# Kernel tuning notes

Hardware: AMD Instinct MI355X
Metric: run time of the kernel (lower is better)

Reference implementation:

```python
import jax, jax.numpy as jnp
import numpy as np

D_MAIN = 256
D_INT = 512
N_FEAT = 128
N_CLASSES = 10
B = 1024
N_CAND = 100000
CTX = 96
EPS = 1e-5


def layer_norm(x, scale, bias):
    m = jnp.mean(x, axis=-1, keepdims=True)
    v = jnp.var(x, axis=-1, keepdims=True)
    return (x - m) / jnp.sqrt(v + EPS) * scale + bias


def setup_inputs() -> dict:
    key = jax.random.key(0)
    ks = jax.random.split(key, 16)

    def lin_w(k, fi, fo):
        return jax.random.uniform(k, (fi, fo), minval=-1.0, maxval=1.0, dtype=jnp.float32) / np.sqrt(fi)

    def lin_b(k, fi, fo):
        return jax.random.uniform(k, (fo,), minval=-1.0, maxval=1.0, dtype=jnp.float32) / np.sqrt(fi)

    return {
        "x_num": jax.random.normal(ks[0], (B, N_FEAT), dtype=jnp.float32),
        "cand_num": jax.random.normal(ks[1], (N_CAND, N_FEAT), dtype=jnp.float32),
        "cand_y": jax.random.randint(ks[2], (N_CAND,), 0, N_CLASSES),
        "context_size": CTX,
        # input linear (forward_E with encoder_n_blocks=0)
        "W_lin": lin_w(ks[3], N_FEAT, D_MAIN), "b_lin": lin_b(ks[3], N_FEAT, D_MAIN),
        # K projection
        "W_K": lin_w(ks[4], D_MAIN, D_MAIN), "b_K": lin_b(ks[4], D_MAIN, D_MAIN),
        # label embedding Y (init uniform(-1, 1) per reset_parameters)
        "Y_emb": jax.random.uniform(ks[5], (N_CLASSES, D_MAIN), minval=-1.0, maxval=1.0, dtype=jnp.float32),
        # T: Linear(d, d_int) -> ReLU -> Linear(d_int, d, bias=False)
        "T_W1": lin_w(ks[6], D_MAIN, D_INT), "T_b1": lin_b(ks[6], D_MAIN, D_INT),
        "T_W2": lin_w(ks[7], D_INT, D_MAIN),
        # predictor block (LayerNorm -> Linear -> ReLU -> Dropout -> Linear), residual
        "bp_ln_s": jnp.ones((D_MAIN,), jnp.float32), "bp_ln_b": jnp.zeros((D_MAIN,), jnp.float32),
        "bp_W1": lin_w(ks[8], D_MAIN, D_INT), "bp_b1": lin_b(ks[8], D_MAIN, D_INT),
        "bp_W2": lin_w(ks[9], D_INT, D_MAIN), "bp_b2": lin_b(ks[9], D_INT, D_MAIN),
        # head P: LayerNorm -> ReLU -> Linear(d, n_classes)
        "P_ln_s": jnp.ones((D_MAIN,), jnp.float32), "P_ln_b": jnp.zeros((D_MAIN,), jnp.float32),
        "P_W": lin_w(ks[10], D_MAIN, N_CLASSES), "P_b": lin_b(ks[10], D_MAIN, N_CLASSES),
    }


def reference(x_num, cand_num, cand_y, context_size,
              W_lin, b_lin, W_K, b_K, Y_emb, T_W1, T_b1, T_W2,
              bp_ln_s, bp_ln_b, bp_W1, bp_b1, bp_W2, bp_b2,
              P_ln_s, P_ln_b, P_W, P_b):
    # forward_E (encoder_n_blocks=0 => single Linear, normlization is None)
    x = x_num @ W_lin + b_lin                       # [B, d]
    k = x @ W_K + b_K                               # [B, d]

    # candidate keys computed under torch.no_grad in the original -> stop_gradient
    ki_all = jax.lax.stop_gradient((cand_num @ W_lin + b_lin) @ W_K + b_K)  # [N, d]

    # FAISS GpuIndexFlatL2 search: exact L2 top-k (smallest squared distance)
    d2 = (jnp.sum(k * k, axis=-1, keepdims=True)
          - 2.0 * (k @ ki_all.T)
          + jnp.sum(ki_all * ki_all, axis=-1))      # [B, N]
    _, I = jax.lax.top_k(-jax.lax.stop_gradient(d2), context_size)  # [B, C]

    ki = ki_all[I]                                  # [B, C, d]
    diff = k[:, None, :] - ki                       # [B, C, d]
    # NOTE: source computes S = -(-|k|^2 + 2 k.ki - |ki|^2) = +squared distance
    S = jnp.sum(diff * diff, axis=-1)               # [B, C]
    w = jax.nn.softmax(S, axis=-1)                  # context_dropout inactive at inference

    enc_y = Y_emb[cand_y[I]]                        # [B, C, d]
    V = enc_y + jax.nn.relu(diff @ T_W1 + T_b1) @ T_W2
    V = jnp.einsum('bc,bcd->bd', w, V)              # weighted aggregation

    x = x + V
    # predictor block (predictor_n_blocks=1)
    h = layer_norm(x, bp_ln_s, bp_ln_b)
    h = jax.nn.relu(h @ bp_W1 + bp_b1) @ bp_W2 + bp_b2
    x = x + h
    # head P
    return jax.nn.relu(layer_norm(x, P_ln_s, P_ln_b)) @ P_W + P_b
```

## Files before the change

### kernel.cpp

```cpp
#include <hip/hip_runtime.h>
#include <hip/hip_bf16.h>

#define B_ROWS   1024
#define N_FEAT   128
#define D_MAIN   256
#define D_INT    512
#define N_CAND   100000
#define CTX      96
#define N_CLS    10
#define PCHN     8192
#define N2       91808
#define RKEEP    128
#define SCAP     6144
#define SVSTRIDE 16

typedef __attribute__((ext_vector_type(8))) short bf16x8;
typedef __attribute__((ext_vector_type(4))) float f32x4;
typedef unsigned long long u64;

__device__ __forceinline__ float wsum(float v) {
    #pragma unroll
    for (int o = 32; o > 0; o >>= 1) v += __shfl_down(v, o);
    return v;
}
__device__ __forceinline__ float wmax(float v) {
    #pragma unroll
    for (int o = 32; o > 0; o >>= 1) v = fmaxf(v, __shfl_down(v, o));
    return v;
}
__device__ __forceinline__ float blockSum256(float v, float* red) {
    int t = threadIdx.x;
    float s = wsum(v);
    if ((t & 63) == 0) red[t >> 6] = s;
    __syncthreads();
    s = red[0] + red[1] + red[2] + red[3];
    __syncthreads();
    return s;
}
__device__ __forceinline__ float b2f(unsigned short u) {
    return __uint_as_float(((unsigned)u) << 16);
}
__device__ __forceinline__ unsigned short f2b(float f) {
    unsigned x = __float_as_uint(f);
    return (unsigned short)((x + 0x7fff + ((x >> 16) & 1)) >> 16);
}
__device__ __forceinline__ unsigned fkey(float f) {
    unsigned u = __float_as_uint(f);
    return u ^ ((((int)u >> 31)) | 0x80000000u);
}
__device__ __forceinline__ float finv(unsigned k) {
    unsigned u = (k & 0x80000000u) ? (k ^ 0x80000000u) : ~k;
    return __uint_as_float(u);
}
#define SPLIT1(x, hv, lv) { unsigned short _h = f2b(x); hv = (short)_h; lv = (short)f2b((x) - b2f(_h)); }

__global__ __launch_bounds__(256) void encode_batch(
    const float* __restrict__ xn, const float* __restrict__ Wl, const float* __restrict__ bl,
    const float* __restrict__ Wk, const float* __restrict__ bk,
    float* __restrict__ xout, float* __restrict__ kout, float* __restrict__ knorm)
{
    int b = blockIdx.x, t = threadIdx.x;
    __shared__ float si[128], sx[256], red[4];
    if (t < 128) si[t] = xn[b * N_FEAT + t];
    __syncthreads();
    float a = bl[t];
    for (int i = 0; i < 128; ++i) a += si[i] * Wl[i * D_MAIN + t];
    xout[b * D_MAIN + t] = a;
    sx[t] = a;
    __syncthreads();
    float a2 = bk[t];
    for (int i = 0; i < 256; ++i) a2 += sx[i] * Wk[i * D_MAIN + t];
    kout[b * D_MAIN + t] = a2;
    float s = blockSum256(a2 * a2, red);
    if (t == 0) knorm[b] = s;
}

__global__ __launch_bounds__(256) void fuse_weights(
    const float* __restrict__ Wl, const float* __restrict__ Wk,
    const float* __restrict__ bl, const float* __restrict__ bk,
    float* __restrict__ Wf, float* __restrict__ bf)
{
    int i = blockIdx.x, t = threadIdx.x;
    __shared__ float row[256];
    if (i < 128) {
        row[t] = Wl[i * D_MAIN + t];
        __syncthreads();
        float a = 0.f;
        for (int k = 0; k < 256; ++k) a += row[k] * Wk[k * D_MAIN + t];
        Wf[i * D_MAIN + t] = a;
    } else {
        row[t] = bl[t];
        __syncthreads();
        float a = bk[t];
        for (int k = 0; k < 256; ++k) a += row[k] * Wk[k * D_MAIN + t];
        bf[t] = a;
    }
}

template<bool WRITE_BF16>
__global__ __launch_bounds__(256) void gemm_split3(
    const float* __restrict__ A,
    const unsigned short* __restrict__ Bh,
    const unsigned short* __restrict__ Bl,
    const float* __restrict__ bias,
    float* __restrict__ Cf,
    unsigned short* __restrict__ Cbf,
    int M, int N, int K)
{
    __shared__ __align__(16) short Ash[4096], Asl[4096];
    __shared__ __align__(16) short Bsh[2048], Bsl[2048];
    const int t = threadIdx.x;
    const int bm = blockIdx.x * 128, bn = blockIdx.y * 64;
    const int wave = t >> 6, lane = t & 63;
    const int wm = (wave >> 1) * 64, wn = (wave & 1) * 32;
    const int lr = lane & 15, lkg = lane >> 4;
    f32x4 acc[4][2] = {};
    const int row0 = t >> 2, kg0 = t & 3;
    const int row1 = row0 + 64;
    const int p0 = ((kg0 + (row0 >> 2)) & 3) ^ (row0 & 3);
    const int p1 = ((kg0 + (row1 >> 2)) & 3) ^ (row1 & 3);
    const int gm0 = bm + row0, gm1 = bm + row1;
    const int nB = bn + row0;

    float4 u00, u01, u10, u11;
    bf16x8 bh0, bl0;
    auto prefetch = [&](int kq) {
        float4 z4 = make_float4(0.f, 0.f, 0.f, 0.f); bf16x8 z = {};
        u00 = z4; u01 = z4; u10 = z4; u11 = z4;
        bh0 = z; bl0 = z;
        if (gm0 < M) {
            const float* ap = A + (size_t)gm0 * K + kq + kg0 * 8;
            u00 = *(const float4*)ap; u01 = *(const float4*)(ap + 4);
        }
        if (gm1 < M) {
            const float* ap = A + (size_t)gm1 * K + kq + kg0 * 8;
            u10 = *(const float4*)ap; u11 = *(const float4*)(ap + 4);
        }
        if (nB < N) {
            bh0 = *(const bf16x8*)(Bh + (size_t)nB * K + kq + kg0 * 8);
            bl0 = *(const bf16x8*)(Bl + (size_t)nB * K + kq + kg0 * 8);
        }
    };
    prefetch(0);

    for (int k0 = 0; k0 < K; k0 += 32) {
        bf16x8 a0h, a0l, a1h, a1l;
        SPLIT1(u00.x, a0h[0], a0l[0]); SPLIT1(u00.y, a0h[1], a0l[1]);
        SPLIT1(u00.z, a0h[2], a0l[2]); SPLIT1(u00.w, a0h[3], a0l[3]);
        SPLIT1(u01.x, a0h[4], a0l[4]); SPLIT1(u01.y, a0h[5], a0l[5]);
        SPLIT1(u01.z, a0h[6], a0l[6]); SPLIT1(u01.w, a0h[7], a0l[7]);
        SPLIT1(u10.x, a1h[0], a1l[0]); SPLIT1(u10.y, a1h[1], a1l[1]);
        SPLIT1(u10.z, a1h[2], a1l[2]); SPLIT1(u10.w, a1h[3], a1l[3]);
        SPLIT1(u11.x, a1h[4], a1l[4]); SPLIT1(u11.y, a1h[5], a1l[5]);
        SPLIT1(u11.z, a1h[6], a1l[6]); SPLIT1(u11.w, a1h[7], a1l[7]);
        __syncthreads();
        *(bf16x8*)&Ash[(row0 * 4 + p0) * 8] = a0h;
        *(bf16x8*)&Asl[(row0 * 4 + p0) * 8] = a0l;
        *(bf16x8*)&Ash[(row1 * 4 + p1) * 8] = a1h;
        *(bf16x8*)&Asl[(row1 * 4 + p1) * 8] = a1l;
        *(bf16x8*)&Bsh[(row0 * 4 + p0) * 8] = bh0;
        *(bf16x8*)&Bsl[(row0 * 4 + p0) * 8] = bl0;
        if (k0 + 32 < K) prefetch(k0 + 32);
        __syncthreads();
        bf16x8 bfh[2], bfl[2];
        #pragma unroll
        for (int n = 0; n < 2; ++n) {
            int r = wn + n * 16 + lr;
            int p = ((lkg + (r >> 2)) & 3) ^ (r & 3);
            bfh[n] = *(const bf16x8*)&Bsh[(r * 4 + p) * 8];
            bfl[n] = *(const bf16x8*)&Bsl[(r * 4 + p) * 8];
        }
        #pragma unroll
        for (int m = 0; m < 4; ++m) {
            int r = wm + m * 16 + lr;
            int p = ((lkg + (r >> 2)) & 3) ^ (r & 3);
            bf16x8 ah = *(const bf16x8*)&Ash[(r * 4 + p) * 8];
            bf16x8 al = *(const bf16x8*)&Asl[(r * 4 + p) * 8];
            #pragma unroll
            for (int n = 0; n < 2; ++n) {
                acc[m][n] = __builtin_amdgcn_mfma_f32_16x16x32_bf16(al, bfh[n], acc[m][n], 0, 0, 0);
                acc[m][n] = __builtin_amdgcn_mfma_f32_16x16x32_bf16(ah, bfl[n], acc[m][n], 0, 0, 0);
                acc[m][n] = __builtin_amdgcn_mfma_f32_16x16x32_bf16(ah, bfh[n], acc[m][n], 0, 0, 0);
            }
        }
    }
    #pragma unroll
    for (int m = 0; m < 4; ++m) {
        #pragma unroll
        for (int n = 0; n < 2; ++n) {
            f32x4 a = acc[m][n];
            int gcol = bn + wn + n * 16 + lr;
            if (gcol >= N) continue;
            float bv = bias[gcol];
            #pragma unroll
            for (int r = 0; r < 4; ++r) {
                int grow = bm + wm + m * 16 + lkg * 4 + r;
                if (grow >= M) continue;
                float v = a[r] + bv;
                Cf[(size_t)grow * N + gcol] = v;
                if (WRITE_BF16) Cbf[(size_t)grow * N + gcol] = f2b(v);
            }
        }
    }
}

template<bool RELU, bool OUT_BF16>
__global__ __launch_bounds__(256) void gemm_bf16(
    const unsigned short* __restrict__ A,
    const unsigned short* __restrict__ Bt,
    const float* __restrict__ bias,
    void* __restrict__ C, int M, int N, int K)
{
    __shared__ __align__(16) short As[2][4096];
    __shared__ __align__(16) short Bs[2][2048];
    const int t = threadIdx.x;
    const int bm = blockIdx.x * 128, bn = blockIdx.y * 64;
    const int wave = t >> 6, lane = t & 63;
    const int wm = (wave >> 1) * 64, wn = (wave & 1) * 32;
    const int lr = lane & 15, lkg = lane >> 4;
    f32x4 acc[4][2] = {};
    const int row0 = t >> 2, kg0 = t & 3;
    const int row1 = row0 + 64;
    const int p0 = ((kg0 + (row0 >> 2)) & 3) ^ (row0 & 3);
    const int p1 = ((kg0 + (row1 >> 2)) & 3) ^ (row1 & 3);
    const int gm0 = bm + row0, gm1 = bm + row1;
    const int nB = bn + row0;

    bf16x8 a0, a1, b0;
    auto prefetch = [&](int kq) {
        bf16x8 z = {};
        a0 = z; a1 = z; b0 = z;
        if (gm0 < M) a0 = *(const bf16x8*)(A + (size_t)gm0 * K + kq + kg0 * 8);
        if (gm1 < M) a1 = *(const bf16x8*)(A + (size_t)gm1 * K + kq + kg0 * 8);
        if (nB < N) b0 = *(const bf16x8*)(Bt + (size_t)nB * K + kq + kg0 * 8);
    };
    prefetch(0);
    *(bf16x8*)&As[0][(row0 * 4 + p0) * 8] = a0;
    *(bf16x8*)&As[0][(row1 * 4 + p1) * 8] = a1;
    *(bf16x8*)&Bs[0][(row0 * 4 + p0) * 8] = b0;
    if (32 < K) prefetch(32);
    __syncthreads();

    for (int k0 = 0; k0 < K; k0 += 32) {
        const int cur = (k0 >> 5) & 1;
        if (k0 + 32 < K) {
            const int nxt = cur ^ 1;
            *(bf16x8*)&As[nxt][(row0 * 4 + p0) * 8] = a0;
            *(bf16x8*)&As[nxt][(row1 * 4 + p1) * 8] = a1;
            *(bf16x8*)&Bs[nxt][(row0 * 4 + p0) * 8] = b0;
            if (k0 + 64 < K) prefetch(k0 + 64);
        }
        bf16x8 bfr[2];
        #pragma unroll
        for (int n = 0; n < 2; ++n) {
            int r = wn + n * 16 + lr;
            int p = ((lkg + (r >> 2)) & 3) ^ (r & 3);
            bfr[n] = *(const bf16x8*)&Bs[cur][(r * 4 + p) * 8];
        }
        #pragma unroll
        for (int m = 0; m < 4; ++m) {
            int r = wm + m * 16 + lr;
            int p = ((lkg + (r >> 2)) & 3) ^ (r & 3);
            bf16x8 af = *(const bf16x8*)&As[cur][(r * 4 + p) * 8];
            #pragma unroll
            for (int n = 0; n < 2; ++n)
                acc[m][n] = __builtin_amdgcn_mfma_f32_16x16x32_bf16(
                    af, bfr[n], acc[m][n], 0, 0, 0);
        }
        __syncthreads();
    }
    #pragma unroll
    for (int m = 0; m < 4; ++m) {
        #pragma unroll
        for (int n = 0; n < 2; ++n) {
            f32x4 a = acc[m][n];
            int gcol = bn + wn + n * 16 + lr;
            if (gcol >= N) continue;
            float bv = bias ? bias[gcol] : 0.f;
            #pragma unroll
            for (int r = 0; r < 4; ++r) {
                int grow = bm + wm + m * 16 + lkg * 4 + r;
                if (grow >= M) continue;
                float v = a[r] + bv;
                if (RELU) v = fmaxf(v, 0.f);
                if (OUT_BF16)
                    ((unsigned short*)C)[(size_t)grow * N + gcol] = f2b(v);
                else
                    ((float*)C)[(size_t)grow * N + gcol] = v;
            }
        }
    }
}

template<int MODE>
__global__ __launch_bounds__(256) void screen_gemm(
    const unsigned short* __restrict__ A,
    const unsigned short* __restrict__ Bt,
    float* __restrict__ scores,
    int N, int n0,
    const float* __restrict__ knrm,
    const unsigned* __restrict__ tau32, int* __restrict__ svcnt,
    u64* __restrict__ surv)
{
    __shared__ __align__(16) short As[2][4096];
    __shared__ __align__(16) short Bs[2][2048];
    const int t = threadIdx.x;
    const int bm = blockIdx.x * 128, bn = blockIdx.y * 64;
    const int wave = t >> 6, lane = t & 63;
    const int wm = (wave >> 1) * 64, wn = (wave & 1) * 32;
    const int lr = lane & 15, lkg = lane >> 4;
    f32x4 acc[4][2] = {};
    const int row0 = t >> 2, kg0 = t & 3;
    const int row1 = row0 + 64;
    const int p0 = ((kg0 + (row0 >> 2)) & 3) ^ (row0 & 3);
    const int p1 = ((kg0 + (row1 >> 2)) & 3) ^ (row1 & 3);
    const int gm0 = bm + row0, gm1 = bm + row1;
    const int nB = bn + row0;

    bf16x8 a0, a1, b0;
    auto prefetch = [&](int kq) {
        bf16x8 z = {};
        b0 = z;
        a0 = *(const bf16x8*)(A + (size_t)gm0 * D_MAIN + kq + kg0 * 8);
        a1 = *(const bf16x8*)(A + (size_t)gm1 * D_MAIN + kq + kg0 * 8);
        if (nB < N) b0 = *(const bf16x8*)(Bt + (size_t)nB * D_MAIN + kq + kg0 * 8);
    };
    prefetch(0);
    *(bf16x8*)&As[0][(row0 * 4 + p0) * 8] = a0;
    *(bf16x8*)&As[0][(row1 * 4 + p1) * 8] = a1;
    *(bf16x8*)&Bs[0][(row0 * 4 + p0) * 8] = b0;
    prefetch(32);
    __syncthreads();

    for (int k0 = 0; k0 < D_MAIN; k0 += 32) {
        const int cur = (k0 >> 5) & 1;
        if (k0 + 32 < D_MAIN) {
            const int nxt = cur ^ 1;
            *(bf16x8*)&As[nxt][(row0 * 4 + p0) * 8] = a0;
            *(bf16x8*)&As[nxt][(row1 * 4 + p1) * 8] = a1;
            *(bf16x8*)&Bs[nxt][(row0 * 4 + p0) * 8] = b0;
            if (k0 + 64 < D_MAIN) prefetch(k0 + 64);
        }
        bf16x8 bfr[2];
        #pragma unroll
        for (int n = 0; n < 2; ++n) {
            int r = wn + n * 16 + lr;
            int p = ((lkg + (r >> 2)) & 3) ^ (r & 3);
            bfr[n] = *(const bf16x8*)&Bs[cur][(r * 4 + p) * 8];
        }
        #pragma unroll
        for (int m = 0; m < 4; ++m) {
            int r = wm + m * 16 + lr;
            int p = ((lkg + (r >> 2)) & 3) ^ (r & 3);
            bf16x8 af = *(const bf16x8*)&As[cur][(r * 4 + p) * 8];
            #pragma unroll
            for (int n = 0; n < 2; ++n)
                acc[m][n] = __builtin_amdgcn_mfma_f32_16x16x32_bf16(
                    af, bfr[n], acc[m][n], 0, 0, 0);
        }
        __syncthreads();
    }

    float knv[2];
    #pragma unroll
    for (int n = 0; n < 2; ++n) {
        int gcol = bn + wn + n * 16 + lr;
        knv[n] = (gcol < N) ? knrm[gcol] : 0.f;
    }
    if (MODE == 1) {
        #pragma unroll
        for (int m = 0; m < 4; ++m) {
            #pragma unroll
            for (int n = 0; n < 2; ++n) {
                int gcol = bn + wn + n * 16 + lr;
                if (gcol >= N) continue;
                #pragma unroll
                for (int r = 0; r < 4; ++r) {
                    int grow = bm + wm + m * 16 + lkg * 4 + r;
                    scores[(size_t)grow * PCHN + gcol] = knv[n] - 2.0f * acc[m][n][r];
                }
            }
        }
    } else {
        unsigned taur[16];
        #pragma unroll
        for (int m = 0; m < 4; ++m)
            #pragma unroll
            for (int r = 0; r < 4; ++r)
                taur[m * 4 + r] = tau32[bm + wm + m * 16 + lkg * 4 + r];
        #pragma unroll
        for (int m = 0; m < 4; ++m) {
            #pragma unroll
            for (int r = 0; r < 4; ++r) {
                int grow = bm + wm + m * 16 + lkg * 4 + r;
                #pragma unroll
                for (int n = 0; n < 2; ++n) {
                    int gcol = bn + wn + n * 16 + lr;
                    bool pass = false;
                    unsigned key = 0;
                    if (gcol < N) {
                        key = fkey(knv[n] - 2.0f * acc[m][n][r]);
                        pass = key <= taur[m * 4 + r];
                    }
                    u64 bal = __ballot(pass);
                    unsigned g16 = (unsigned)((bal >> (lkg * 16)) & 0xFFFFu);
                    if (g16) {
                        int cntp = __popc(g16);
                        int first = __ffs(g16) - 1;
                        int base = 0;
                        if (lr == first) base = atomicAdd(&svcnt[grow * SVSTRIDE], cntp);
                        base = __shfl(base, lkg * 16 + first);
                        if (pass) {
                            int p = base + __popc(g16 & ((1u << lr) - 1u));
                            if (p < SCAP)
                                surv[(size_t)grow * SCAP + p] =
                                    ((u64)key << 32) | (unsigned)(n0 + gcol);
                        }
                    }
                }
            }
        }
    }
}

__global__ __launch_bounds__(256) void cvt_f32_bf16_vec(
    const float* __restrict__ in, unsigned short* __restrict__ out, int n4)
{
    int i = blockIdx.x * 256 + threadIdx.x;
    if (i >= n4) return;
    float4 v = ((const float4*)in)[i];
    ushort4 u;
    u.x = f2b(v.x); u.y = f2b(v.y); u.z = f2b(v.z); u.w = f2b(v.w);
    ((ushort4*)out)[i] = u;
}
__global__ __launch_bounds__(256) void cvt_transpose(
    const float* __restrict__ W, unsigned short* __restrict__ Wt, int K, int N)
{
    int idx = blockIdx.x * 256 + threadIdx.x;
    if (idx >= K * N) return;
    int k = idx / N, n = idx % N;
    Wt[(size_t)n * K + k] = f2b(W[idx]);
}
__global__ __launch_bounds__(256) void cvt_split_transpose(
    const float* __restrict__ W, unsigned short* __restrict__ Wh,
    unsigned short* __restrict__ Wl, int K, int N)
{
    int idx = blockIdx.x * 256 + threadIdx.x;
    if (idx >= K * N) return;
    int k = idx / N, n = idx % N;
    float v = W[idx];
    unsigned short h = f2b(v);
    Wh[(size_t)n * K + k] = h;
    Wl[(size_t)n * K + k] = f2b(v - b2f(h));
}

__global__ __launch_bounds__(256) void rownorms(const float* __restrict__ ki,
                                                float* __restrict__ out, int M)
{
    int n = blockIdx.x * 4 + (threadIdx.x >> 6);
    int lane = threadIdx.x & 63;
    if (n >= M) return;
    float4 v = *(const float4*)(ki + (size_t)n * D_MAIN + lane * 4);
    float s = v.x * v.x + v.y * v.y + v.z * v.z + v.w * v.w;
    s = wsum(s);
    if (lane == 0) out[n] = s;
}

__device__ void bitonic512(u64* s, int t)
{
    for (int k = 2; k <= 512; k <<= 1) {
        for (int j = k >> 1; j > 0; j >>= 1) {
            __syncthreads();
            #pragma unroll
            for (int q = 0; q < 2; ++q) {
                int l = t + q * 256;
                int p = l ^ j;
                if (p > l) {
                    u64 a = s[l], bb = s[p];
                    bool up = ((l & k) == 0);
                    if ((a > bb) == up) { s[l] = bb; s[p] = a; }
                }
            }
        }
    }
    __syncthreads();
}
__device__ void bitonic1024(u64* s, int t)
{
    for (int k = 2; k <= 1024; k <<= 1) {
        for (int j = k >> 1; j > 0; j >>= 1) {
            __syncthreads();
            #pragma unroll
            for (int q = 0; q < 4; ++q) {
                int l = t + q * 256;
                int p = l ^ j;
                if (p > l) {
                    u64 a = s[l], bb = s[p];
                    bool up = ((l & k) == 0);
                    if ((a > bb) == up) { s[l] = bb; s[p] = a; }
                }
            }
        }
    }
    __syncthreads();
}

__global__ __launch_bounds__(256) void pilot_select(
    const float* __restrict__ scores, u64* __restrict__ pilotbuf,
    unsigned* __restrict__ tau32)
{
    int b = blockIdx.x, t = threadIdx.x;
    int lane = t & 63;
    __shared__ u64 s[1024];
    __shared__ int cnt;
    __shared__ u64 tauf;
    const float* row = scores + (size_t)b * PCHN;
    #pragma unroll
    for (int q = 0; q < 4; ++q) {
        int n = t + q * 256;
        s[n] = ((u64)fkey(row[n]) << 32) | (unsigned)n;
    }
    __syncthreads();
    bitonic1024(s, t);
    if (t == 0) { cnt = 128; tauf = s[127]; }
    #pragma unroll
    for (int q = 0; q < 4; ++q) { int n = t + q * 256; if (n >= 128) s[n] = ~0ULL; }
    __syncthreads();
    for (int base = 1024; base < PCHN; base += 1024) {
        u64 tau = tauf;
        int n = base + t * 4;
        float4 v = *(const float4*)(row + n);
        #pragma unroll
        for (int j = 0; j < 4; ++j) {
            float x = (&v.x)[j];
            u64 e = ((u64)fkey(x) << 32) | (unsigned)(n + j);
            bool pass = e < tau;
            u64 m = __ballot(pass);
            if (m) {
                int bs = 0;
                if (lane == 0) bs = atomicAdd(&cnt, (int)__popcll(m));
                bs = __shfl(bs, 0);
                if (pass) {
                    int p = bs + (int)__popcll(m & ((1ULL << lane) - 1ULL));
                    if (p < 1024) s[p] = e;
                }
            }
        }
        __syncthreads();
        if (cnt > 512) {
            bitonic1024(s, t);
            if (t == 0) { cnt = 128; tauf = s[127]; }
            #pragma unroll
            for (int q = 0; q < 4; ++q) { int n2 = t + q * 256; if (n2 >= 128) s[n2] = ~0ULL; }
        }
        __syncthreads();
    }
    bitonic1024(s, t);
    if (t < 128) pilotbuf[(size_t)b * 128 + t] = s[t];
    if (t == 0) tau32[b] = (unsigned)(s[127] >> 32);
}

__global__ __launch_bounds__(128) void init_surv(
    const u64* __restrict__ pilotbuf, u64* __restrict__ surv, int* __restrict__ svcnt)
{
    int b = blockIdx.x, t = threadIdx.x;
    surv[(size_t)b * SCAP + t] = pilotbuf[(size_t)b * 128 + t];
    if (t == 0) svcnt[b * SVSTRIDE] = 128;
}

__global__ __launch_bounds__(256) void final_select(
    const u64* __restrict__ surv, const int* __restrict__ svcnt,
    int* __restrict__ refI)
{
    int b = blockIdx.x, t = threadIdx.x;
    int lane = t & 63;
    __shared__ u64 s[1024];
    __shared__ int cnt;
    __shared__ u64 tauf;
    int total = svcnt[b * SVSTRIDE]; if (total > SCAP) total = SCAP;
    const u64* rowp = surv + (size_t)b * SCAP;
    #pragma unroll
    for (int q = 0; q < 4; ++q) {
        int n = t + q * 256;
        s[n] = (n < total) ? rowp[n] : ~0ULL;
    }
    __syncthreads();
    bitonic1024(s, t);
    if (t == 0) { cnt = 128; tauf = s[127]; }
    #pragma unroll
    for (int q = 0; q < 4; ++q) { int n = t + q * 256; if (n >= 128) s[n] = ~0ULL; }
    __syncthreads();
    for (int base = 1024; base < total; base += 1024) {
        u64 tau = tauf;
        int n = base + t * 4;
        #pragma unroll
        for (int j = 0; j < 4; ++j) {
            u64 e = (n + j < total) ? rowp[n + j] : ~0ULL;
            bool pass = e < tau;
            u64 m = __ballot(pass);
            if (m) {
                int bs = 0;
                if (lane == 0) bs = atomicAdd(&cnt, (int)__popcll(m));
                bs = __shfl(bs, 0);
                if (pass) {
                    int p = bs + (int)__popcll(m & ((1ULL << lane) - 1ULL));
                    if (p < 1024) s[p] = e;
                }
            }
        }
        __syncthreads();
        if (cnt > 512) {
            bitonic1024(s, t);
            if (t == 0) { cnt = 128; tauf = s[127]; }
            #pragma unroll
            for (int q = 0; q < 4; ++q) { int n2 = t + q * 256; if (n2 >= 128) s[n2] = ~0ULL; }
        }
        __syncthreads();
    }
    bitonic1024(s, t);
    if (t < RKEEP) refI[b * RKEEP + t] = (int)(unsigned)(s[t] & 0xffffffffULL);
}

__global__ __launch_bounds__(256) void refine(
    const float* __restrict__ kmat, const float* __restrict__ kiall,
    const float* __restrict__ knorm, const float* __restrict__ kinorm,
    const int* __restrict__ refI, int* __restrict__ Ifin, float* __restrict__ Sbuf)
{
    int b = blockIdx.x, t = threadIdx.x;
    int w = t >> 6, lane = t & 63;
    __shared__ float kk[256];
    __shared__ u64 s[512];
    kk[t] = kmat[b * D_MAIN + t];
    s[t] = ~0ULL; s[t + 256] = ~0ULL;
    __syncthreads();
    float kn = knorm[b];
    for (int sv = w; sv < RKEEP; sv += 4) {
        int n = refI[b * RKEEP + sv];
        float4 a = *(const float4*)&kk[lane * 4];
        float4 bb = ((const float4*)(kiall + (size_t)n * D_MAIN))[lane];
        float d = a.x * bb.x + a.y * bb.y + a.z * bb.z + a.w * bb.w;
        d = wsum(d);
        if (lane == 0) {
            float d2 = kn + kinorm[n] - 2.f * d;
            s[sv] = ((u64)fkey(d2) << 32) | (unsigned)n;
        }
    }
    __syncthreads();
    bitonic512(s, t);
    if (t < CTX) {
        u64 e = s[t];
        Ifin[b * CTX + t] = (int)(unsigned)(e & 0xffffffffULL);
        Sbuf[b * CTX + t] = finv((unsigned)(e >> 32));
    }
}

__global__ __launch_bounds__(64) void gather_diff_bf(
    const float* __restrict__ kmat, const float* __restrict__ kiall,
    const int* __restrict__ I, unsigned short* __restrict__ diffb)
{
    int bc = blockIdx.x;
    int b = bc / CTX;
    int t = threadIdx.x;
    int idx = I[bc];
    float4 kv = ((const float4*)(kmat + (size_t)b * D_MAIN))[t];
    float4 iv = ((const float4*)(kiall + (size_t)idx * D_MAIN))[t];
    ushort4 u;
    u.x = f2b(kv.x - iv.x); u.y = f2b(kv.y - iv.y);
    u.z = f2b(kv.z - iv.z); u.w = f2b(kv.w - iv.w);
    ((ushort4*)(diffb + (size_t)bc * D_MAIN))[t] = u;
}

__global__ __launch_bounds__(128) void softmax96(const float* __restrict__ S,
                                                 float* __restrict__ w)
{
    int b = blockIdx.x, t = threadIdx.x;
    __shared__ float rm[2], rs[2];
    float v = (t < CTX) ? S[b * CTX + t] : -__builtin_inff();
    float m = wmax(v);
    if ((t & 63) == 0) rm[t >> 6] = m;
    __syncthreads();
    m = fmaxf(rm[0], rm[1]);
    float e = (t < CTX) ? expf(v - m) : 0.f;
    float ss = wsum(e);
    if ((t & 63) == 0) rs[t >> 6] = ss;
    __syncthreads();
    float Z = rs[0] + rs[1];
    if (t < CTX) w[b * CTX + t] = e / Z;
}

__global__ __launch_bounds__(256) void aggregate(
    const float* __restrict__ w, const int* __restrict__ I,
    const int* __restrict__ cand_y, const float* __restrict__ Yemb,
    const float* __restrict__ mlp, const float* __restrict__ x,
    float* __restrict__ x2)
{
    int b = blockIdx.x, t = threadIdx.x;
    __shared__ float ws[CTX];
    __shared__ int lab[CTX];
    if (t < CTX) {
        ws[t] = w[b * CTX + t];
        lab[t] = cand_y[I[b * CTX + t]];
    }
    __syncthreads();
    float acc = 0.f;
    for (int c = 0; c < CTX; ++c) {
        acc += ws[c] * (Yemb[lab[c] * D_MAIN + t] + mlp[((size_t)b * CTX + c) * D_MAIN + t]);
    }
    x2[b * D_MAIN + t] = x[b * D_MAIN + t] + acc;
}

__global__ __launch_bounds__(256) void predictor_head(
    const float* __restrict__ x2,
    const float* __restrict__ lns, const float* __restrict__ lnb,
    const float* __restrict__ W1, const float* __restrict__ b1,
    const float* __restrict__ W2, const float* __restrict__ b2,
    const float* __restrict__ plns, const float* __restrict__ plnb,
    const float* __restrict__ PW, const float* __restrict__ Pb,
    float* __restrict__ out)
{
    int b = blockIdx.x, t = threadIdx.x;
    __shared__ float ln1[256], hdn[512], red[4];
    float xv = x2[b * D_MAIN + t];
    float s1 = blockSum256(xv, red);
    float s2 = blockSum256(xv * xv, red);
    float mean = s1 * (1.f / 256.f);
    float var = s2 * (1.f / 256.f) - mean * mean;
    float rstd = rsqrtf(var + 1e-5f);
    ln1[t] = (xv - mean) * rstd * lns[t] + lnb[t];
    __syncthreads();
    #pragma unroll
    for (int rep = 0; rep < 2; ++rep) {
        int j = t + rep * 256;
        float a = b1[j];
        for (int i = 0; i < 256; ++i) a += ln1[i] * W1[i * D_INT + j];
        hdn[j] = fmaxf(a, 0.f);
    }
    __syncthreads();
    float a3 = b2[t];
    for (int i = 0; i < 512; ++i) a3 += hdn[i] * W2[i * D_MAIN + t];
    float x3 = xv + a3;
    float s3 = blockSum256(x3, red);
    float s4 = blockSum256(x3 * x3, red);
    float m2 = s3 * (1.f / 256.f);
    float v2 = s4 * (1.f / 256.f) - m2 * m2;
    float r2 = rsqrtf(v2 + 1e-5f);
    float rv = fmaxf((x3 - m2) * r2 * plns[t] + plnb[t], 0.f);
    __syncthreads();
    ln1[t] = rv;
    __syncthreads();
    if (t < N_CLS) {
        float a = Pb[t];
        for (int i = 0; i < 256; ++i) a += ln1[i] * PW[i * N_CLS + t];
        out[b * N_CLS + t] = a;
    }
}

extern "C" void kernel_launch(void* const* d_in, const int* in_sizes, int n_in,
                              void* d_out, int out_size, void* d_ws, size_t ws_size,
                              hipStream_t stream)
{
    (void)in_sizes; (void)n_in; (void)out_size; (void)ws_size;
    const float* x_num   = (const float*)d_in[0];
    const float* cand    = (const float*)d_in[1];
    const int*   cand_y  = (const int*)d_in[2];
    const float* W_lin   = (const float*)d_in[4];
    const float* b_lin   = (const float*)d_in[5];
    const float* W_K     = (const float*)d_in[6];
    const float* b_K     = (const float*)d_in[7];
    const float* Y_emb   = (const float*)d_in[8];
    const float* T_W1    = (const float*)d_in[9];
    const float* T_b1    = (const float*)d_in[10];
    const float* T_W2    = (const float*)d_in[11];
    const float* bp_ln_s = (const float*)d_in[12];
    const float* bp_ln_b = (const float*)d_in[13];
    const float* bp_W1   = (const float*)d_in[14];
    const float* bp_b1   = (const float*)d_in[15];
    const float* bp_W2   = (const float*)d_in[16];
    const float* bp_b2   = (const float*)d_in[17];
    const float* P_ln_s  = (const float*)d_in[18];
    const float* P_ln_b  = (const float*)d_in[19];
    const float* P_W     = (const float*)d_in[20];
    const float* P_b     = (const float*)d_in[21];
    float* outp = (float*)d_out;

    char* ws = (char*)d_ws;
    float* kiall  = (float*)(ws + 0);
    unsigned short* hidden = (unsigned short*)(ws + 0);
    unsigned short* ki_bf = (unsigned short*)(ws + 102400000);
    unsigned short* diffb = (unsigned short*)(ws + 102400000);
    float* mlpbuf = (float*)(ws + 102400000);
    float* scores = (float*)(ws + 153600000);
    u64*   surv   = (u64*)(ws + 153600000);
    const size_t T = 204800000;
    float* xbuf   = (float*)(ws + T + 0);
    float* kbuf   = (float*)(ws + T + 1048576);
    float* x2buf  = (float*)(ws + T + 2097152);
    float* knorm  = (float*)(ws + T + 3145728);
    float* kinorm = (float*)(ws + T + 3149824);
    unsigned short* k_bf = (unsigned short*)(ws + T + 3551232);
    float* Wf     = (float*)(ws + T + 4075520);
    unsigned short* WfH = (unsigned short*)(ws + T + 4206592);
    unsigned short* WfL = (unsigned short*)(ws + T + 4272128);
    float* bfused = (float*)(ws + T + 4337664);
    unsigned short* W1t  = (unsigned short*)(ws + T + 4468736);
    unsigned short* W2t  = (unsigned short*)(ws + T + 4730880);
    float* Sbuf   = (float*)(ws + T + 4993024);
    float* wbuf   = (float*)(ws + T + 5386240);
    int*   refI   = (int*)(ws + T + 5779456);
    int*   Ifin   = (int*)(ws + T + 6303744);
    u64*   pilotbuf = (u64*)(ws + T + 6696960);
    unsigned* tau32 = (unsigned*)(ws + T + 7745536);
    int*   svcnt  = (int*)(ws + T + 7749632);

    encode_batch<<<B_ROWS, 256, 0, stream>>>(x_num, W_lin, b_lin, W_K, b_K,
                                             xbuf, kbuf, knorm);
    fuse_weights<<<129, 256, 0, stream>>>(W_lin, W_K, b_lin, b_K, Wf, bfused);
    cvt_split_transpose<<<128, 256, 0, stream>>>(Wf, WfH, WfL, N_FEAT, D_MAIN);
    cvt_transpose<<<512, 256, 0, stream>>>(T_W1, W1t, D_MAIN, D_INT);
    cvt_transpose<<<512, 256, 0, stream>>>(T_W2, W2t, D_INT, D_MAIN);
    cvt_f32_bf16_vec<<<256, 256, 0, stream>>>(kbuf, k_bf, B_ROWS * D_MAIN / 4);
    gemm_split3<true><<<dim3(782, 4), 256, 0, stream>>>(
        cand, WfH, WfL, bfused, kiall, ki_bf, N_CAND, D_MAIN, N_FEAT);
    rownorms<<<25000, 256, 0, stream>>>(kiall, kinorm, N_CAND);
    screen_gemm<1><<<dim3(8, PCHN / 64), 256, 0, stream>>>(
        k_bf, ki_bf, scores, PCHN, 0, kinorm, nullptr, nullptr, nullptr);
    pilot_select<<<B_ROWS, 256, 0, stream>>>(scores, pilotbuf, tau32);
    init_surv<<<B_ROWS, 128, 0, stream>>>(pilotbuf, surv, svcnt);
    screen_gemm<2><<<dim3(8, (N2 + 63) / 64), 256, 0, stream>>>(
        k_bf, ki_bf + (size_t)PCHN * D_MAIN, nullptr, N2, PCHN,
        kinorm + PCHN, tau32, svcnt, surv);
    final_select<<<B_ROWS, 256, 0, stream>>>(surv, svcnt, refI);
    refine<<<B_ROWS, 256, 0, stream>>>(kbuf, kiall, knorm, kinorm, refI, Ifin, Sbuf);
    softmax96<<<B_ROWS, 128, 0, stream>>>(Sbuf, wbuf);
    gather_diff_bf<<<B_ROWS * CTX, 64, 0, stream>>>(kbuf, kiall, Ifin, diffb);
    gemm_bf16<true, true><<<dim3(768, 8), 256, 0, stream>>>(
        diffb, W1t, T_b1, hidden, B_ROWS * CTX, D_INT, D_MAIN);
    gemm_bf16<false, false><<<dim3(768, 4), 256, 0, stream>>>(
        hidden, W2t, nullptr, mlpbuf, B_ROWS * CTX, D_MAIN, D_INT);
    aggregate<<<B_ROWS, 256, 0, stream>>>(wbuf, Ifin, cand_y, Y_emb, mlpbuf,
                                          xbuf, x2buf);
    predictor_head<<<B_ROWS, 256, 0, stream>>>(x2buf, bp_ln_s, bp_ln_b,
                                               bp_W1, bp_b1, bp_W2, bp_b2,
                                               P_ln_s, P_ln_b, P_W, P_b, outp);
}
```

Measured before the change: 802.1 us.

## Stage GEMM tiles via direct global-to-LDS async loads

Replaces the register-staged prefetch and LDS store in both the generic bf16 GEMM and the screening GEMM with global_load_lds 16-byte direct transfers. An inverse-swizzle mapping picks each lane's source chunk so the existing swizzled LDS layout stays the same. This is meant to cut VGPR pressure and the LDS write instructions in the main loop. Out-of-bounds guards on M/N are dropped, so partial tiles (e.g. the candidate tail) may read past the array end. Whether the async loads are properly waited on before the barrier is also uncertain.

```diff
diff --git a/kernel.cpp b/kernel.cpp
--- a/kernel.cpp
+++ b/kernel.cpp
@@ -51,6 +51,13 @@
 __device__ __forceinline__ float finv(unsigned k) {
     unsigned u = (k & 0x80000000u) ? (k ^ 0x80000000u) : ~k;
     return __uint_as_float(u);
+}
+__device__ __forceinline__ void async16(const unsigned short* g, short* l) {
+    __builtin_amdgcn_global_load_lds((const unsigned int*)g, (unsigned int*)l, 16, 0, 0);
+}
+__device__ __forceinline__ int inv_kg(int s) {
+    int g = s >> 2;
+    return (((s & 3) ^ (g & 3)) - (g >> 2)) & 3;
 }
 #define SPLIT1(x, hv, lv) { unsigned short _h = f2b(x); hv = (short)_h; lv = (short)f2b((x) - b2f(_h)); }
 
@@ -219,37 +226,24 @@
     const int wm = (wave >> 1) * 64, wn = (wave & 1) * 32;
     const int lr = lane & 15, lkg = lane >> 4;
     f32x4 acc[4][2] = {};
-    const int row0 = t >> 2, kg0 = t & 3;
-    const int row1 = row0 + 64;
-    const int p0 = ((kg0 + (row0 >> 2)) & 3) ^ (row0 & 3);
-    const int p1 = ((kg0 + (row1 >> 2)) & 3) ^ (row1 & 3);
-    const int gm0 = bm + row0, gm1 = bm + row1;
-    const int nB = bn + row0;
-
-    bf16x8 a0, a1, b0;
-    auto prefetch = [&](int kq) {
-        bf16x8 z = {};
-        a0 = z; a1 = z; b0 = z;
-        if (gm0 < M) a0 = *(const bf16x8*)(A + (size_t)gm0 * K + kq + kg0 * 8);
-        if (gm1 < M) a1 = *(const bf16x8*)(A + (size_t)gm1 * K + kq + kg0 * 8);
-        if (nB < N) b0 = *(const bf16x8*)(Bt + (size_t)nB * K + kq + kg0 * 8);
+
+    const int sA0 = wave * 128 + lane, sA1 = sA0 + 64, sB = wave * 64 + lane;
+    const unsigned short* srcA0 = A + (size_t)(bm + (sA0 >> 2)) * K + inv_kg(sA0) * 8;
+    const unsigned short* srcA1 = A + (size_t)(bm + (sA1 >> 2)) * K + inv_kg(sA1) * 8;
+    const unsigned short* srcB  = Bt + (size_t)(bn + (sB >> 2)) * K + inv_kg(sB) * 8;
+
+    auto stage = [&](int buf, int kq) {
+        async16(srcA0 + kq, &As[buf][(wave * 128) * 8]);
+        async16(srcA1 + kq, &As[buf][(wave * 128 + 64) * 8]);
+        async16(srcB + kq, &Bs[buf][(wave * 64) * 8]);
     };
-    prefetch(0);
-    *(bf16x8*)&As[0][(row0 * 4 + p0) * 8] = a0;
-    *(bf16x8*)&As[0][(row1 * 4 + p1) * 8] = a1;
-    *(bf16x8*)&Bs[0][(row0 * 4 + p0) * 8] = b0;
-    if (32 < K) prefetch(32);
-    __syncthreads();
-
-    for (int k0 = 0; k0 < K; k0 += 32) {
-        const int cur = (k0 >> 5) & 1;
-        if (k0 + 32 < K) {
-            const int nxt = cur ^ 1;
-            *(bf16x8*)&As[nxt][(row0 * 4 + p0) * 8] = a0;
-            *(bf16x8*)&As[nxt][(row1 * 4 + p1) * 8] = a1;
-            *(bf16x8*)&Bs[nxt][(row0 * 4 + p0) * 8] = b0;
-            if (k0 + 64 < K) prefetch(k0 + 64);
-        }
+    stage(0, 0);
+    __syncthreads();
+
+    const int nsteps = K >> 5;
+    for (int s = 0; s < nsteps; ++s) {
+        const int cur = s & 1;
+        if (s + 1 < nsteps) stage(cur ^ 1, (s + 1) << 5);
         bf16x8 bfr[2];
         #pragma unroll
         for (int n = 0; n < 2; ++n) {
@@ -310,37 +304,23 @@
     const int wm = (wave >> 1) * 64, wn = (wave & 1) * 32;
     const int lr = lane & 15, lkg = lane >> 4;
     f32x4 acc[4][2] = {};
-    const int row0 = t >> 2, kg0 = t & 3;
-    const int row1 = row0 + 64;
-    const int p0 = ((kg0 + (row0 >> 2)) & 3) ^ (row0 & 3);
-    const int p1 = ((kg0 + (row1 >> 2)) & 3) ^ (row1 & 3);
-    const int gm0 = bm + row0, gm1 = bm + row1;
-    const int nB = bn + row0;
-
-    bf16x8 a0, a1, b0;
-    auto prefetch = [&](int kq) {
-        bf16x8 z = {};
-        b0 = z;
-        a0 = *(const bf16x8*)(A + (size_t)gm0 * D_MAIN + kq + kg0 * 8);
-        a1 = *(const bf16x8*)(A + (size_t)gm1 * D_MAIN + kq + kg0 * 8);
-        if (nB < N) b0 = *(const bf16x8*)(Bt + (size_t)nB * D_MAIN + kq + kg0 * 8);
+
+    const int sA0 = wave * 128 + lane, sA1 = sA0 + 64, sB = wave * 64 + lane;
+    const unsigned short* srcA0 = A + (size_t)(bm + (sA0 >> 2)) * D_MAIN + inv_kg(sA0) * 8;
+    const unsigned short* srcA1 = A + (size_t)(bm + (sA1 >> 2)) * D_MAIN + inv_kg(sA1) * 8;
+    const unsigned short* srcB  = Bt + (size_t)(bn + (sB >> 2)) * D_MAIN + inv_kg(sB) * 8;
+
+    auto stage = [&](int buf, int kq) {
+        async16(srcA0 + kq, &As[buf][(wave * 128) * 8]);
+        async16(srcA1 + kq, &As[buf][(wave * 128 + 64) * 8]);
+        async16(srcB + kq, &Bs[buf][(wave * 64) * 8]);
     };
-    prefetch(0);
-    *(bf16x8*)&As[0][(row0 * 4 + p0) * 8] = a0;
-    *(bf16x8*)&As[0][(row1 * 4 + p1) * 8] = a1;
-    *(bf16x8*)&Bs[0][(row0 * 4 + p0) * 8] = b0;
-    prefetch(32);
-    __syncthreads();
-
-    for (int k0 = 0; k0 < D_MAIN; k0 += 32) {
-        const int cur = (k0 >> 5) & 1;
-        if (k0 + 32 < D_MAIN) {
-            const int nxt = cur ^ 1;
-            *(bf16x8*)&As[nxt][(row0 * 4 + p0) * 8] = a0;
-            *(bf16x8*)&As[nxt][(row1 * 4 + p1) * 8] = a1;
-            *(bf16x8*)&Bs[nxt][(row0 * 4 + p0) * 8] = b0;
-            if (k0 + 64 < D_MAIN) prefetch(k0 + 64);
-        }
+    stage(0, 0);
+    __syncthreads();
+
+    for (int s = 0; s < 8; ++s) {
+        const int cur = s & 1;
+        if (s + 1 < 8) stage(cur ^ 1, (s + 1) << 5);
         bf16x8 bfr[2];
         #pragma unroll
         for (int n = 0; n < 2; ++n) {
```

Result: slower. 827.3 us (+3.1%).

## Load screen GEMM fragments directly from global memory, fuse bf16 cast of k

Applied to the files above, without the earlier changes.

The screen GEMM drops its LDS double-buffered staging. Each wave now loads its MFMA fragments straight from global memory into registers with a two-stage register prefetch, and a block covers 256 rows by 32 columns instead of 128 by 64. Bounds checks go away because N2 and PCHN are multiples of 32. The separate fp32-to-bf16 conversion kernel for k is removed and the cast is written out in encode_batch. The aim is to cut LDS traffic and barrier stalls, at the cost of more redundant global and L2 reads of the B tile across waves.

```diff
diff --git a/kernel.cpp b/kernel.cpp
--- a/kernel.cpp
+++ b/kernel.cpp
@@ -57,7 +57,8 @@
 __global__ __launch_bounds__(256) void encode_batch(
     const float* __restrict__ xn, const float* __restrict__ Wl, const float* __restrict__ bl,
     const float* __restrict__ Wk, const float* __restrict__ bk,
-    float* __restrict__ xout, float* __restrict__ kout, float* __restrict__ knorm)
+    float* __restrict__ xout, float* __restrict__ kout, float* __restrict__ knorm,
+    unsigned short* __restrict__ kbf)
 {
     int b = blockIdx.x, t = threadIdx.x;
     __shared__ float si[128], sx[256], red[4];
@@ -71,6 +72,7 @@
     float a2 = bk[t];
     for (int i = 0; i < 256; ++i) a2 += sx[i] * Wk[i * D_MAIN + t];
     kout[b * D_MAIN + t] = a2;
+    kbf[b * D_MAIN + t] = f2b(a2);
     float s = blockSum256(a2 * a2, red);
     if (t == 0) knorm[b] = s;
 }
@@ -302,81 +304,56 @@
     const unsigned* __restrict__ tau32, int* __restrict__ svcnt,
     u64* __restrict__ surv)
 {
-    __shared__ __align__(16) short As[2][4096];
-    __shared__ __align__(16) short Bs[2][2048];
     const int t = threadIdx.x;
-    const int bm = blockIdx.x * 128, bn = blockIdx.y * 64;
     const int wave = t >> 6, lane = t & 63;
-    const int wm = (wave >> 1) * 64, wn = (wave & 1) * 32;
     const int lr = lane & 15, lkg = lane >> 4;
+    const int bm = (blockIdx.x * 4 + wave) * 64;
+    const int bn = blockIdx.y * 32;
     f32x4 acc[4][2] = {};
-    const int row0 = t >> 2, kg0 = t & 3;
-    const int row1 = row0 + 64;
-    const int p0 = ((kg0 + (row0 >> 2)) & 3) ^ (row0 & 3);
-    const int p1 = ((kg0 + (row1 >> 2)) & 3) ^ (row1 & 3);
-    const int gm0 = bm + row0, gm1 = bm + row1;
-    const int nB = bn + row0;
-
-    bf16x8 a0, a1, b0;
-    auto prefetch = [&](int kq) {
-        bf16x8 z = {};
-        b0 = z;
-        a0 = *(const bf16x8*)(A + (size_t)gm0 * D_MAIN + kq + kg0 * 8);
-        a1 = *(const bf16x8*)(A + (size_t)gm1 * D_MAIN + kq + kg0 * 8);
-        if (nB < N) b0 = *(const bf16x8*)(Bt + (size_t)nB * D_MAIN + kq + kg0 * 8);
-    };
-    prefetch(0);
-    *(bf16x8*)&As[0][(row0 * 4 + p0) * 8] = a0;
-    *(bf16x8*)&As[0][(row1 * 4 + p1) * 8] = a1;
-    *(bf16x8*)&Bs[0][(row0 * 4 + p0) * 8] = b0;
-    prefetch(32);
-    __syncthreads();
-
-    for (int k0 = 0; k0 < D_MAIN; k0 += 32) {
-        const int cur = (k0 >> 5) & 1;
-        if (k0 + 32 < D_MAIN) {
-            const int nxt = cur ^ 1;
-            *(bf16x8*)&As[nxt][(row0 * 4 + p0) * 8] = a0;
-            *(bf16x8*)&As[nxt][(row1 * 4 + p1) * 8] = a1;
-            *(bf16x8*)&Bs[nxt][(row0 * 4 + p0) * 8] = b0;
-            if (k0 + 64 < D_MAIN) prefetch(k0 + 64);
-        }
-        bf16x8 bfr[2];
-        #pragma unroll
-        for (int n = 0; n < 2; ++n) {
-            int r = wn + n * 16 + lr;
-            int p = ((lkg + (r >> 2)) & 3) ^ (r & 3);
-            bfr[n] = *(const bf16x8*)&Bs[cur][(r * 4 + p) * 8];
-        }
-        #pragma unroll
-        for (int m = 0; m < 4; ++m) {
-            int r = wm + m * 16 + lr;
-            int p = ((lkg + (r >> 2)) & 3) ^ (r & 3);
-            bf16x8 af = *(const bf16x8*)&As[cur][(r * 4 + p) * 8];
+
+    const unsigned short* srcA0 = A + (size_t)(bm + 0 * 16 + lr) * D_MAIN + lkg * 8;
+    const unsigned short* srcA1 = A + (size_t)(bm + 1 * 16 + lr) * D_MAIN + lkg * 8;
+    const unsigned short* srcA2 = A + (size_t)(bm + 2 * 16 + lr) * D_MAIN + lkg * 8;
+    const unsigned short* srcA3 = A + (size_t)(bm + 3 * 16 + lr) * D_MAIN + lkg * 8;
+    const unsigned short* srcB0 = Bt + (size_t)(bn + 0 * 16 + lr) * D_MAIN + lkg * 8;
+    const unsigned short* srcB1 = Bt + (size_t)(bn + 1 * 16 + lr) * D_MAIN + lkg * 8;
+
+    bf16x8 af[2][4], bfg[2][2];
+    #define LOADST(buf, s_) {                                   \
+        af[buf][0] = *(const bf16x8*)(srcA0 + (s_) * 32);       \
+        af[buf][1] = *(const bf16x8*)(srcA1 + (s_) * 32);       \
+        af[buf][2] = *(const bf16x8*)(srcA2 + (s_) * 32);       \
+        af[buf][3] = *(const bf16x8*)(srcA3 + (s_) * 32);       \
+        bfg[buf][0] = *(const bf16x8*)(srcB0 + (s_) * 32);      \
+        bfg[buf][1] = *(const bf16x8*)(srcB1 + (s_) * 32); }
+    LOADST(0, 0);
+    LOADST(1, 1);
+    #pragma unroll
+    for (int s = 0; s < 8; ++s) {
+        const int cur = s & 1;
+        #pragma unroll
+        for (int m = 0; m < 4; ++m)
             #pragma unroll
             for (int n = 0; n < 2; ++n)
                 acc[m][n] = __builtin_amdgcn_mfma_f32_16x16x32_bf16(
-                    af, bfr[n], acc[m][n], 0, 0, 0);
-        }
-        __syncthreads();
-    }
+                    af[cur][m], bfg[cur][n], acc[m][n], 0, 0, 0);
+        if (s + 2 < 8) LOADST(cur, s + 2);
+    }
+    #undef LOADST
 
     float knv[2];
     #pragma unroll
-    for (int n = 0; n < 2; ++n) {
-        int gcol = bn + wn + n * 16 + lr;
-        knv[n] = (gcol < N) ? knrm[gcol] : 0.f;
-    }
+    for (int n = 0; n < 2; ++n) knv[n] = knrm[bn + n * 16 + lr];
+
     if (MODE == 1) {
         #pragma unroll
         for (int m = 0; m < 4; ++m) {
             #pragma unroll
             for (int n = 0; n < 2; ++n) {
-                int gcol = bn + wn + n * 16 + lr;
-                if (gcol >= N) continue;
+                int gcol = bn + n * 16 + lr;
                 #pragma unroll
                 for (int r = 0; r < 4; ++r) {
-                    int grow = bm + wm + m * 16 + lkg * 4 + r;
+                    int grow = bm + m * 16 + lkg * 4 + r;
                     scores[(size_t)grow * PCHN + gcol] = knv[n] - 2.0f * acc[m][n][r];
                 }
             }
@@ -387,21 +364,17 @@
         for (int m = 0; m < 4; ++m)
             #pragma unroll
             for (int r = 0; r < 4; ++r)
-                taur[m * 4 + r] = tau32[bm + wm + m * 16 + lkg * 4 + r];
+                taur[m * 4 + r] = tau32[bm + m * 16 + lkg * 4 + r];
         #pragma unroll
         for (int m = 0; m < 4; ++m) {
             #pragma unroll
             for (int r = 0; r < 4; ++r) {
-                int grow = bm + wm + m * 16 + lkg * 4 + r;
+                int grow = bm + m * 16 + lkg * 4 + r;
                 #pragma unroll
                 for (int n = 0; n < 2; ++n) {
-                    int gcol = bn + wn + n * 16 + lr;
-                    bool pass = false;
-                    unsigned key = 0;
-                    if (gcol < N) {
-                        key = fkey(knv[n] - 2.0f * acc[m][n][r]);
-                        pass = key <= taur[m * 4 + r];
-                    }
+                    int gcol = bn + n * 16 + lr;
+                    unsigned key = fkey(knv[n] - 2.0f * acc[m][n][r]);
+                    bool pass = key <= taur[m * 4 + r];
                     u64 bal = __ballot(pass);
                     unsigned g16 = (unsigned)((bal >> (lkg * 16)) & 0xFFFFu);
                     if (g16) {
@@ -423,16 +396,6 @@
     }
 }
 
-__global__ __launch_bounds__(256) void cvt_f32_bf16_vec(
-    const float* __restrict__ in, unsigned short* __restrict__ out, int n4)
-{
-    int i = blockIdx.x * 256 + threadIdx.x;
-    if (i >= n4) return;
-    float4 v = ((const float4*)in)[i];
-    ushort4 u;
-    u.x = f2b(v.x); u.y = f2b(v.y); u.z = f2b(v.z); u.w = f2b(v.w);
-    ((ushort4*)out)[i] = u;
-}
 __global__ __launch_bounds__(256) void cvt_transpose(
     const float* __restrict__ W, unsigned short* __restrict__ Wt, int K, int N)
 {
@@ -813,20 +776,19 @@
     int*   svcnt  = (int*)(ws + T + 7749632);
 
     encode_batch<<<B_ROWS, 256, 0, stream>>>(x_num, W_lin, b_lin, W_K, b_K,
-                                             xbuf, kbuf, knorm);
+                                             xbuf, kbuf, knorm, k_bf);
     fuse_weights<<<129, 256, 0, stream>>>(W_lin, W_K, b_lin, b_K, Wf, bfused);
     cvt_split_transpose<<<128, 256, 0, stream>>>(Wf, WfH, WfL, N_FEAT, D_MAIN);
     cvt_transpose<<<512, 256, 0, stream>>>(T_W1, W1t, D_MAIN, D_INT);
     cvt_transpose<<<512, 256, 0, stream>>>(T_W2, W2t, D_INT, D_MAIN);
-    cvt_f32_bf16_vec<<<256, 256, 0, stream>>>(kbuf, k_bf, B_ROWS * D_MAIN / 4);
     gemm_split3<true><<<dim3(782, 4), 256, 0, stream>>>(
         cand, WfH, WfL, bfused, kiall, ki_bf, N_CAND, D_MAIN, N_FEAT);
     rownorms<<<25000, 256, 0, stream>>>(kiall, kinorm, N_CAND);
-    screen_gemm<1><<<dim3(8, PCHN / 64), 256, 0, stream>>>(
+    screen_gemm<1><<<dim3(4, PCHN / 32), 256, 0, stream>>>(
         k_bf, ki_bf, scores, PCHN, 0, kinorm, nullptr, nullptr, nullptr);
     pilot_select<<<B_ROWS, 256, 0, stream>>>(scores, pilotbuf, tau32);
     init_surv<<<B_ROWS, 128, 0, stream>>>(pilotbuf, surv, svcnt);
-    screen_gemm<2><<<dim3(8, (N2 + 63) / 64), 256, 0, stream>>>(
+    screen_gemm<2><<<dim3(4, N2 / 32), 256, 0, stream>>>(
         k_bf, ki_bf + (size_t)PCHN * D_MAIN, nullptr, N2, PCHN,
         kinorm + PCHN, tau32, svcnt, surv);
     final_select<<<B_ROWS, 256, 0, stream>>>(surv, svcnt, refI);
```

Result: slower. 929.8 us (+15.9%).
